# Performance work log

Hardware: AMD Instinct MI355X
Metric: run time of the kernel (lower is better)

Reference implementation:

```python
import jax, jax.numpy as jnp
import numpy as np

D_MODEL = 1024
D_FF = 4096
N_EXPERTS = 8
TOP_K = 2
TEMP = 0.7
B, L = 4, 2048


def setup_inputs() -> dict:
    key = jax.random.key(0)
    ks = jax.random.split(key, 6)
    s = 0.02  # init scale
    return {
        "x": jax.random.normal(ks[0], (B, L, D_MODEL), jnp.float32),
        "Wr": jax.random.normal(ks[1], (D_MODEL, N_EXPERTS), jnp.float32) * s,
        "br": jnp.zeros((N_EXPERTS,), jnp.float32),
        "W1": jax.random.normal(ks[2], (N_EXPERTS, D_MODEL, D_FF), jnp.float32) * s,
        "b1": jnp.zeros((N_EXPERTS, D_FF), jnp.float32),
        "W2": jax.random.normal(ks[3], (N_EXPERTS, D_FF, D_MODEL), jnp.float32) * s,
        "b2": jnp.zeros((N_EXPERTS, D_MODEL), jnp.float32),
    }


def reference(x, Wr, br, W1, b1, W2, b2):
    # Eval-mode MoE: no router jitter, dropout is identity.
    Bb, Ll, Dd = x.shape
    E = Wr.shape[1]
    xf = x.reshape(-1, Dd)                              # [T, D]
    T = xf.shape[0]

    logits = xf @ Wr + br                               # [T, E]
    probs = jax.nn.softmax(logits / TEMP, axis=-1)      # [T, E]
    top_w, top_i = jax.lax.top_k(probs, TOP_K)          # [T, K]
    top_w = top_w / (jnp.sum(top_w, axis=-1, keepdims=True) + 1e-6)

    # Per-token per-expert combine weight (zero for non-selected experts).
    cw = jnp.zeros((T, E), xf.dtype).at[jnp.arange(T)[:, None], top_i].add(top_w)

    out = jnp.zeros_like(xf)
    for e in range(E):  # small fixed expert loop
        h = jax.nn.silu(xf @ W1[e] + b1[e])             # [T, d_ff]
        out = out + cw[:, e:e + 1] * (h @ W2[e] + b2[e])

    # Load-balance aux loss.
    counts = jnp.zeros((E,), xf.dtype).at[top_i.reshape(-1)].add(1.0)
    f_i = counts / T
    P_i = probs.mean(axis=0)
    aux = E * jnp.sum(f_i * P_i)
    return out.reshape(Bb, Ll, Dd), aux[None]
```

## Files before the change

kernel.cpp:

```cpp
#include <hip/hip_runtime.h>

#define DM     1024
#define DFF    4096
#define NE     8
#define TT     8192
#define CAP    8192
#define RTOK   32
#define MAXRA  17664

typedef __bf16 bf16x8 __attribute__((ext_vector_type(8)));
typedef float  f32x4  __attribute__((ext_vector_type(4)));
typedef unsigned short u16;
typedef unsigned int   u32;

__device__ __forceinline__ u16 f2bf(float f) {
    u32 u = __builtin_bit_cast(u32, f);
    u += 0x7fffu + ((u >> 16) & 1u);
    return (u16)(u >> 16);
}

__device__ __forceinline__ void gload_lds16(const void* g, void* l) {
    __builtin_amdgcn_global_load_lds(
        (const __attribute__((address_space(1))) void*)g,
        (__attribute__((address_space(3))) void*)l,
        16, 0, 0);
}

__global__ __launch_bounds__(256) void router_k(
    const float* __restrict__ x, const float* __restrict__ Wr, const float* __restrict__ br,
    int* __restrict__ expert_count, float* __restrict__ prob_sum,
    int* __restrict__ list_token, float* __restrict__ list_w,
    int* __restrict__ tok_e, int* __restrict__ tok_q, float* __restrict__ tok_w)
{
    __shared__ float wrT[NE][DM];
    __shared__ float ps[NE];
    __shared__ int   lcount[NE];
    __shared__ int   lbase[NE];
    __shared__ int   lexp[RTOK * 2];
    __shared__ float lw[RTOK * 2];
    __shared__ int   lslot[RTOK * 2];

    int tid = threadIdx.x;
    if (tid < NE) { ps[tid] = 0.f; lcount[tid] = 0; }
#pragma unroll
    for (int it = 0; it < 8; ++it) {
        int f = tid * 4 + it * 1024;
        float4 v = *reinterpret_cast<const float4*>(Wr + f);
        int e0 = f & 7, k = f >> 3;
        wrT[e0][k] = v.x; wrT[e0 + 1][k] = v.y; wrT[e0 + 2][k] = v.z; wrT[e0 + 3][k] = v.w;
    }
    __syncthreads();

    int w = tid >> 6, l = tid & 63;
    for (int j = 0; j < RTOK / 4; ++j) {
        int ti = w * (RTOK / 4) + j;
        int token = blockIdx.x * RTOK + ti;
        const float* xr = x + (size_t)token * DM;
        float acc[NE];
#pragma unroll
        for (int e = 0; e < NE; ++e) acc[e] = 0.f;
#pragma unroll
        for (int i = 0; i < 4; ++i) {
            float4 xv = *reinterpret_cast<const float4*>(xr + i * 256 + l * 4);
#pragma unroll
            for (int e = 0; e < NE; ++e) {
                float4 wv = *reinterpret_cast<const float4*>(&wrT[e][i * 256 + l * 4]);
                acc[e] += xv.x * wv.x + xv.y * wv.y + xv.z * wv.z + xv.w * wv.w;
            }
        }
#pragma unroll
        for (int off = 32; off >= 1; off >>= 1) {
#pragma unroll
            for (int e = 0; e < NE; ++e) acc[e] += __shfl_xor(acc[e], off);
        }
        if (l == 0) {
            float li[NE], m = -1e30f;
#pragma unroll
            for (int e = 0; e < NE; ++e) { li[e] = (acc[e] + br[e]) * (1.0f / 0.7f); m = fmaxf(m, li[e]); }
            float p[NE], s = 0.f;
#pragma unroll
            for (int e = 0; e < NE; ++e) { p[e] = __expf(li[e] - m); s += p[e]; }
            float inv = 1.f / s;
#pragma unroll
            for (int e = 0; e < NE; ++e) { p[e] *= inv; atomicAdd(&ps[e], p[e]); }
            float v1 = -1.f, v2 = -1.f; int e1 = 0, e2 = 0;
#pragma unroll
            for (int e = 0; e < NE; ++e) {
                float pe = p[e];
                if (pe > v1)      { v2 = v1; e2 = e1; v1 = pe; e1 = e; }
                else if (pe > v2) { v2 = pe; e2 = e; }
            }
            float denom = v1 + v2 + 1e-6f;
            lexp[2 * ti]     = e1; lw[2 * ti]     = v1 / denom; lslot[2 * ti]     = atomicAdd(&lcount[e1], 1);
            lexp[2 * ti + 1] = e2; lw[2 * ti + 1] = v2 / denom; lslot[2 * ti + 1] = atomicAdd(&lcount[e2], 1);
        }
    }
    __syncthreads();
    if (tid < NE) {
        lbase[tid] = atomicAdd(&expert_count[tid], lcount[tid]);
        atomicAdd(&prob_sum[tid], ps[tid]);
    }
    __syncthreads();
    if (tid < RTOK * 2) {
        int e = lexp[tid];
        int q = lbase[e] + lslot[tid];
        int token = blockIdx.x * RTOK + (tid >> 1);
        list_token[e * CAP + q] = token;
        list_w[e * CAP + q] = lw[tid];
        int slot = token * 2 + (tid & 1);
        tok_e[slot] = e; tok_q[slot] = q; tok_w[slot] = lw[tid];
    }
}

__global__ void scan_aux_k(const int* __restrict__ expert_count, const float* __restrict__ prob_sum,
                           int* __restrict__ padded_count, int* __restrict__ poffsets,
                           float* __restrict__ aux_out)
{
    if (threadIdx.x == 0 && blockIdx.x == 0) {
        int off = 0; float aux = 0.f;
        for (int e = 0; e < NE; ++e) {
            int c = expert_count[e];
            int pc = (c + 127) / 128 * 128;
            poffsets[e] = off; padded_count[e] = pc; off += pc;
            aux += ((float)c / (float)TT) * (prob_sum[e] / (float)TT);
        }
        aux_out[0] = aux * (float)NE;
    }
}

__global__ __launch_bounds__(256) void gather_k(
    const float* __restrict__ x, const int* __restrict__ list_token,
    const int* __restrict__ expert_count, const int* __restrict__ padded_count,
    const int* __restrict__ poffsets, u16* __restrict__ Xg)
{
    int e = blockIdx.y;
    int p0 = blockIdx.x * 8;
    if (p0 >= padded_count[e]) return;
    int tid = threadIdx.x;
    int rr = tid >> 5, cl = tid & 31;
    int p = p0 + rr;
    int g = poffsets[e] + p;
    u16* dst = Xg + (size_t)g * DM;
    bool valid = p < expert_count[e];
    int tok = valid ? list_token[e * CAP + p] : 0;
    const float* src = x + (size_t)tok * DM;
#pragma unroll
    for (int i = 0; i < 4; ++i) {
        int c0 = cl * 8 + i * 256;
        uint4 v;
        if (valid) {
            float4 f0 = *reinterpret_cast<const float4*>(src + c0);
            float4 f1 = *reinterpret_cast<const float4*>(src + c0 + 4);
            v.x = f2bf(f0.x) | ((u32)f2bf(f0.y) << 16);
            v.y = f2bf(f0.z) | ((u32)f2bf(f0.w) << 16);
            v.z = f2bf(f1.x) | ((u32)f2bf(f1.y) << 16);
            v.w = f2bf(f1.z) | ((u32)f2bf(f1.w) << 16);
        } else {
            v.x = 0; v.y = 0; v.z = 0; v.w = 0;
        }
        *reinterpret_cast<uint4*>(dst + c0) = v;
    }
}

__global__ __launch_bounds__(256) void convt_k(
    const float* __restrict__ src, u16* __restrict__ dst, int rs, int Ktot, long dstEStride)
{
    __shared__ float tile[64][65];
    int e = blockIdx.z;
    int k0 = blockIdx.x * 64, j0 = blockIdx.y * 64;
    const float* s = src + (size_t)e * 4194304;
    int tid = threadIdx.x;
    {
        int jj = (tid & 15) * 4, kb = tid >> 4;
#pragma unroll
        for (int i = 0; i < 4; ++i) {
            int k = kb + i * 16;
            float4 v = *reinterpret_cast<const float4*>(s + (size_t)(k0 + k) * rs + j0 + jj);
            tile[k][jj] = v.x; tile[k][jj + 1] = v.y; tile[k][jj + 2] = v.z; tile[k][jj + 3] = v.w;
        }
    }
    __syncthreads();
    {
        int kk = (tid & 15) * 4, jb = tid >> 4;
        u16* d = dst + (size_t)e * dstEStride;
#pragma unroll
        for (int i = 0; i < 4; ++i) {
            int j = jb + i * 16;
            uint2 q;
            q.x = f2bf(tile[kk][j])     | ((u32)f2bf(tile[kk + 1][j]) << 16);
            q.y = f2bf(tile[kk + 2][j]) | ((u32)f2bf(tile[kk + 3][j]) << 16);
            *reinterpret_cast<uint2*>(d + (size_t)(j0 + j) * Ktot + k0 + kk) = q;
        }
    }
}

__device__ __forceinline__ void stage_tile(const u16* __restrict__ rows, long lda, int kt, char* buf) {
    int tid = threadIdx.x;
    int w = tid >> 6, l = tid & 63;
#pragma unroll
    for (int i = 0; i < 4; ++i) {
        int sbase = i * 256 + w * 64;
        int sl = sbase + l;
        int row = sl >> 3;
        int c8 = (sl & 7) ^ (row & 7);
        const u16* src = rows + (size_t)row * lda + kt * 64 + c8 * 8;
        gload_lds16(src, buf + sbase * 16);
    }
}

__device__ __forceinline__ void gemm_main(
    const u16* __restrict__ Arows, long lda,
    const u16* __restrict__ Brows, long ldb,
    int nkt, char* smem, f32x4 acc[4][4])
{
    int tid = threadIdx.x;
    int l = tid & 63, lane16 = l & 15, hi = l >> 4;
    int wm = (tid >> 6) & 1, wn = tid >> 7;

    for (int kt = 0; kt < nkt; ++kt) {
        stage_tile(Arows, lda, kt, smem);
        stage_tile(Brows, ldb, kt, smem + 16384);
        __syncthreads();
        const char* bufA = smem;
        const char* bufB = smem + 16384;
#pragma unroll
        for (int kk = 0; kk < 2; ++kk) {
            bf16x8 af[4], bb[4];
#pragma unroll
            for (int mi = 0; mi < 4; ++mi) {
                int row = wm * 64 + mi * 16 + lane16;
                int ch = (kk * 4 + hi) ^ (row & 7);
                af[mi] = *reinterpret_cast<const bf16x8*>(bufA + (row * 8 + ch) * 16);
            }
#pragma unroll
            for (int ni = 0; ni < 4; ++ni) {
                int row = wn * 64 + ni * 16 + lane16;
                int ch = (kk * 4 + hi) ^ (row & 7);
                bb[ni] = *reinterpret_cast<const bf16x8*>(bufB + (row * 8 + ch) * 16);
            }
#pragma unroll
            for (int mi = 0; mi < 4; ++mi)
#pragma unroll
                for (int ni = 0; ni < 4; ++ni)
                    acc[mi][ni] = __builtin_amdgcn_mfma_f32_16x16x32_bf16(af[mi], bb[ni], acc[mi][ni], 0, 0, 0);
        }
        __syncthreads();
    }
}

__global__ __launch_bounds__(256, 4) void gemm1_k(
    const u16* __restrict__ Xg, const u16* __restrict__ W1c, const float* __restrict__ b1,
    const int* __restrict__ padded_count, const int* __restrict__ poffsets,
    u16* __restrict__ H)
{
    __shared__ char smem[32768];
    int n = blockIdx.x;
    int e = n >> 11, r11 = n & 2047;
    int g = r11 >> 8;
    int rb = g * 8 + ((r11 >> 5) & 7);
    int cb = r11 & 31;
    if (rb * 128 >= padded_count[e]) return;
    int row0 = poffsets[e] + rb * 128;
    const u16* Arows = Xg + (size_t)row0 * 1024;
    const u16* Brows = W1c + (size_t)e * DFF * 1024 + (size_t)cb * 128 * 1024;
    f32x4 acc[4][4];
#pragma unroll
    for (int i = 0; i < 4; ++i)
#pragma unroll
        for (int j = 0; j < 4; ++j) { acc[i][j][0]=0.f; acc[i][j][1]=0.f; acc[i][j][2]=0.f; acc[i][j][3]=0.f; }
    gemm_main(Arows, 1024, Brows, 1024, 16, smem, acc);

    int tid = threadIdx.x;
    int l = tid & 63, lane16 = l & 15, hi = l >> 4;
    int wm = (tid >> 6) & 1, wn = tid >> 7;
    const float* b1e = b1 + (size_t)e * DFF;
#pragma unroll
    for (int mi = 0; mi < 4; ++mi) {
#pragma unroll
        for (int ni = 0; ni < 4; ++ni) {
            int col = cb * 128 + wn * 64 + ni * 16 + lane16;
            float bv = b1e[col];
#pragma unroll
            for (int r = 0; r < 4; ++r) {
                int grow = row0 + wm * 64 + mi * 16 + hi * 4 + r;
                float z = acc[mi][ni][r] + bv;
                float hval = z / (1.f + __expf(-z));
                H[(size_t)grow * DFF + col] = f2bf(hval);
            }
        }
    }
}

__global__ __launch_bounds__(256, 4) void gemm2_k(
    const u16* __restrict__ Hb, const u16* __restrict__ W2c,
    const int* __restrict__ padded_count, const int* __restrict__ poffsets,
    float* __restrict__ Og)
{
    __shared__ char smem[32768];
    int n = blockIdx.x;
    int e = n >> 9, r9 = n & 511;
    int g = r9 >> 7;
    int rb = g * 16 + ((r9 >> 3) & 15);
    int cb = r9 & 7;
    if (rb * 128 >= padded_count[e]) return;
    int row0 = poffsets[e] + rb * 128;
    const u16* Arows = Hb + (size_t)row0 * DFF;
    const u16* Brows = W2c + (size_t)e * DM * DFF + (size_t)cb * 128 * DFF;
    f32x4 acc[4][4];
#pragma unroll
    for (int i = 0; i < 4; ++i)
#pragma unroll
        for (int j = 0; j < 4; ++j) { acc[i][j][0]=0.f; acc[i][j][1]=0.f; acc[i][j][2]=0.f; acc[i][j][3]=0.f; }
    gemm_main(Arows, DFF, Brows, DFF, 64, smem, acc);

    int tid = threadIdx.x;
    int l = tid & 63, lane16 = l & 15, hi = l >> 4;
    int wm = (tid >> 6) & 1, wn = tid >> 7;
#pragma unroll
    for (int mi = 0; mi < 4; ++mi) {
#pragma unroll
        for (int r = 0; r < 4; ++r) {
            int grow = row0 + wm * 64 + mi * 16 + hi * 4 + r;
            float* orow = Og + (size_t)grow * DM;
#pragma unroll
            for (int ni = 0; ni < 4; ++ni) {
                int col = cb * 128 + wn * 64 + ni * 16 + lane16;
                orow[col] = acc[mi][ni][r];
            }
        }
    }
}

__global__ __launch_bounds__(256) void combine_k(
    const float* __restrict__ Og, const float* __restrict__ b2,
    const int* __restrict__ tok_e, const int* __restrict__ tok_q, const float* __restrict__ tok_w,
    const int* __restrict__ poffsets, float* __restrict__ out)
{
    int t = blockIdx.x * 4 + (threadIdx.x >> 6);
    int l = threadIdx.x & 63;
    int e0 = tok_e[t * 2], q0 = tok_q[t * 2];
    int e1 = tok_e[t * 2 + 1], q1 = tok_q[t * 2 + 1];
    float w0 = tok_w[t * 2], w1 = tok_w[t * 2 + 1];
    const float* r0 = Og + (size_t)(poffsets[e0] + q0) * DM;
    const float* r1 = Og + (size_t)(poffsets[e1] + q1) * DM;
    const float* bb0 = b2 + (size_t)e0 * DM;
    const float* bb1 = b2 + (size_t)e1 * DM;
    float* o = out + (size_t)t * DM;
#pragma unroll
    for (int i = 0; i < 4; ++i) {
        int c = l * 4 + i * 256;
        float4 a = *reinterpret_cast<const float4*>(r0 + c);
        float4 b = *reinterpret_cast<const float4*>(r1 + c);
        float4 p = *reinterpret_cast<const float4*>(bb0 + c);
        float4 q = *reinterpret_cast<const float4*>(bb1 + c);
        float4 res;
        res.x = w0 * (a.x + p.x) + w1 * (b.x + q.x);
        res.y = w0 * (a.y + p.y) + w1 * (b.y + q.y);
        res.z = w0 * (a.z + p.z) + w1 * (b.z + q.z);
        res.w = w0 * (a.w + p.w) + w1 * (b.w + q.w);
        *reinterpret_cast<float4*>(o + c) = res;
    }
}

extern "C" void kernel_launch(void* const* d_in, const int* in_sizes, int n_in,
                              void* d_out, int out_size, void* d_ws, size_t ws_size,
                              hipStream_t stream) {
    (void)in_sizes; (void)n_in; (void)out_size; (void)ws_size;
    const float* x  = (const float*)d_in[0];
    const float* Wr = (const float*)d_in[1];
    const float* br = (const float*)d_in[2];
    const float* W1 = (const float*)d_in[3];
    const float* b1 = (const float*)d_in[4];
    const float* W2 = (const float*)d_in[5];
    const float* b2 = (const float*)d_in[6];
    float* out = (float*)d_out;

    char* ws = (char*)d_ws;
    int*   expert_count = (int*)(ws + 0);
    float* prob_sum     = (float*)(ws + 32);
    int*   padded_count = (int*)(ws + 64);
    int*   poffsets     = (int*)(ws + 96);
    int*   list_token   = (int*)(ws + 256);
    float* list_w       = (float*)(ws + 256 + 262144);
    int*   tok_e        = (int*)(ws + 524544);
    int*   tok_q        = (int*)(ws + 524544 + 65536);
    float* tok_w        = (float*)(ws + 524544 + 131072);

    const size_t HDR    = 1048576;
    const size_t OFF_HB = HDR;
    const size_t OFF_W2 = OFF_HB + (size_t)MAXRA * DFF * 2;
    const size_t OFF_XG = OFF_W2 + (size_t)NE * DM * DFF * 2;
    const size_t OFF_W1 = OFF_XG + (size_t)MAXRA * DM * 2;
    u16*   Hb  = (u16*)(ws + OFF_HB);
    u16*   W2c = (u16*)(ws + OFF_W2);
    u16*   Xg  = (u16*)(ws + OFF_XG);
    u16*   W1c = (u16*)(ws + OFF_W1);
    float* Og  = (float*)(ws + OFF_XG);

    hipMemsetAsync(ws, 0, 64, stream);
    router_k<<<TT / RTOK, 256, 0, stream>>>(x, Wr, br, expert_count, prob_sum, list_token, list_w,
                                            tok_e, tok_q, tok_w);
    scan_aux_k<<<1, 64, 0, stream>>>(expert_count, prob_sum, padded_count, poffsets,
                                     out + (size_t)TT * DM);
    gather_k<<<dim3(1024, 8), 256, 0, stream>>>(x, list_token, expert_count, padded_count, poffsets, Xg);

    convt_k<<<dim3(16, 64, 8), 256, 0, stream>>>(W1, W1c, DFF, 1024, (long)DM * DFF);
    convt_k<<<dim3(64, 16, 8), 256, 0, stream>>>(W2, W2c, DM, 4096, (long)DM * DFF);

    gemm1_k<<<16384, 256, 0, stream>>>(Xg, W1c, b1, padded_count, poffsets, Hb);
    gemm2_k<<<4096, 256, 0, stream>>>(Hb, W2c, padded_count, poffsets, Og);
    combine_k<<<TT / 4, 256, 0, stream>>>(Og, b2, tok_e, tok_q, tok_w, poffsets, out);
}
```

Baseline: 537.4 us.

## Switch expert GEMMs to 32x32x16 MFMA with 256x128 block tiles

Replaces the 16x16x32 MFMA inner loop with 32x32x16 MFMA instructions. The block tile grows from 128x128 to 256x128, with each wave computing 128x64, which raises operand reuse per LDS read and per global load. The grouped 1D block swizzle becomes a plain 3D grid (col block, row block, expert), and the epilogue gains bounds checks against the padded count. In exchange it uses more LDS and registers (launch bounds drop to 2 blocks per SM), wastes more work on padded rows, and loses the L2-friendly block ordering.

```diff
diff --git a/kernel.cpp b/kernel.cpp
--- a/kernel.cpp
+++ b/kernel.cpp
@@ -9,7 +9,7 @@
 #define MAXRA  17664
 
 typedef __bf16 bf16x8 __attribute__((ext_vector_type(8)));
-typedef float  f32x4  __attribute__((ext_vector_type(4)));
+typedef float  f32x16 __attribute__((ext_vector_type(16)));
 typedef unsigned short u16;
 typedef unsigned int   u32;
 
@@ -194,138 +194,144 @@
     }
 }
 
-__device__ __forceinline__ void stage_tile(const u16* __restrict__ rows, long lda, int kt, char* buf) {
+
+__device__ __forceinline__ f32x16 mfma32(bf16x8 a, bf16x8 b, f32x16 c) {
+    return __builtin_amdgcn_mfma_f32_32x32x16_bf16(a, b, c, 0, 0, 0);
+}
+
+__device__ __forceinline__ void gemm_main32(
+    const u16* __restrict__ A, long lda, const u16* __restrict__ B, long ldb,
+    int nkt, char* smem, f32x16 acc[4][2])
+{
     int tid = threadIdx.x;
-    int w = tid >> 6, l = tid & 63;
-#pragma unroll
-    for (int i = 0; i < 4; ++i) {
-        int sbase = i * 256 + w * 64;
-        int sl = sbase + l;
-        int row = sl >> 3;
-        int c8 = (sl & 7) ^ (row & 7);
-        const u16* src = rows + (size_t)row * lda + kt * 64 + c8 * 8;
-        gload_lds16(src, buf + sbase * 16);
-    }
-}
-
-__device__ __forceinline__ void gemm_main(
-    const u16* __restrict__ Arows, long lda,
-    const u16* __restrict__ Brows, long ldb,
-    int nkt, char* smem, f32x4 acc[4][4])
-{
-    int tid = threadIdx.x;
-    int l = tid & 63, lane16 = l & 15, hi = l >> 4;
-    int wm = (tid >> 6) & 1, wn = tid >> 7;
+    int l = tid & 63, l31 = l & 31, kg = l >> 5;
+    int wid = tid >> 6, wm = wid >> 1, wn = wid & 1;
+    char* bufA = smem;
+    char* bufB = smem + 32768;
 
     for (int kt = 0; kt < nkt; ++kt) {
-        stage_tile(Arows, lda, kt, smem);
-        stage_tile(Brows, ldb, kt, smem + 16384);
+#pragma unroll
+        for (int i = 0; i < 8; ++i) {
+            int sbase = i * 256 + wid * 64;
+            int sl = sbase + l;
+            int row = sl >> 3;
+            int c8 = (sl & 7) ^ (row & 7);
+            gload_lds16(A + (size_t)row * lda + kt * 64 + c8 * 8, bufA + sbase * 16);
+        }
+#pragma unroll
+        for (int i = 0; i < 4; ++i) {
+            int sbase = i * 256 + wid * 64;
+            int sl = sbase + l;
+            int row = sl >> 3;
+            int c8 = (sl & 7) ^ (row & 7);
+            gload_lds16(B + (size_t)row * ldb + kt * 64 + c8 * 8, bufB + sbase * 16);
+        }
         __syncthreads();
-        const char* bufA = smem;
-        const char* bufB = smem + 16384;
-#pragma unroll
-        for (int kk = 0; kk < 2; ++kk) {
-            bf16x8 af[4], bb[4];
+#pragma unroll
+        for (int ks = 0; ks < 4; ++ks) {
+            bf16x8 af[4], bb[2];
 #pragma unroll
             for (int mi = 0; mi < 4; ++mi) {
-                int row = wm * 64 + mi * 16 + lane16;
-                int ch = (kk * 4 + hi) ^ (row & 7);
+                int row = wm * 128 + mi * 32 + l31;
+                int ch = (ks * 2 + kg) ^ (row & 7);
                 af[mi] = *reinterpret_cast<const bf16x8*>(bufA + (row * 8 + ch) * 16);
             }
 #pragma unroll
-            for (int ni = 0; ni < 4; ++ni) {
-                int row = wn * 64 + ni * 16 + lane16;
-                int ch = (kk * 4 + hi) ^ (row & 7);
+            for (int ni = 0; ni < 2; ++ni) {
+                int row = wn * 64 + ni * 32 + l31;
+                int ch = (ks * 2 + kg) ^ (row & 7);
                 bb[ni] = *reinterpret_cast<const bf16x8*>(bufB + (row * 8 + ch) * 16);
             }
 #pragma unroll
             for (int mi = 0; mi < 4; ++mi)
 #pragma unroll
-                for (int ni = 0; ni < 4; ++ni)
-                    acc[mi][ni] = __builtin_amdgcn_mfma_f32_16x16x32_bf16(af[mi], bb[ni], acc[mi][ni], 0, 0, 0);
+                for (int ni = 0; ni < 2; ++ni)
+                    acc[mi][ni] = mfma32(af[mi], bb[ni], acc[mi][ni]);
         }
         __syncthreads();
     }
 }
 
-__global__ __launch_bounds__(256, 4) void gemm1_k(
+__global__ __launch_bounds__(256, 2) void gemm1_k(
     const u16* __restrict__ Xg, const u16* __restrict__ W1c, const float* __restrict__ b1,
     const int* __restrict__ padded_count, const int* __restrict__ poffsets,
     u16* __restrict__ H)
 {
-    __shared__ char smem[32768];
-    int n = blockIdx.x;
-    int e = n >> 11, r11 = n & 2047;
-    int g = r11 >> 8;
-    int rb = g * 8 + ((r11 >> 5) & 7);
-    int cb = r11 & 31;
-    if (rb * 128 >= padded_count[e]) return;
-    int row0 = poffsets[e] + rb * 128;
+    __shared__ char smem[49152];
+    int cb = blockIdx.x, rb = blockIdx.y, e = blockIdx.z;
+    int pc = padded_count[e];
+    if (rb * 256 >= pc) return;
+    int row0 = poffsets[e] + rb * 256;
     const u16* Arows = Xg + (size_t)row0 * 1024;
     const u16* Brows = W1c + (size_t)e * DFF * 1024 + (size_t)cb * 128 * 1024;
-    f32x4 acc[4][4];
+    f32x16 acc[4][2];
 #pragma unroll
     for (int i = 0; i < 4; ++i)
 #pragma unroll
-        for (int j = 0; j < 4; ++j) { acc[i][j][0]=0.f; acc[i][j][1]=0.f; acc[i][j][2]=0.f; acc[i][j][3]=0.f; }
-    gemm_main(Arows, 1024, Brows, 1024, 16, smem, acc);
-
-    int tid = threadIdx.x;
-    int l = tid & 63, lane16 = l & 15, hi = l >> 4;
-    int wm = (tid >> 6) & 1, wn = tid >> 7;
+        for (int j = 0; j < 2; ++j)
+#pragma unroll
+            for (int r = 0; r < 16; ++r) acc[i][j][r] = 0.f;
+    gemm_main32(Arows, 1024, Brows, 1024, 16, smem, acc);
+
+    int tid = threadIdx.x, l = tid & 63, l31 = l & 31, kg = l >> 5;
+    int wid = tid >> 6, wm = wid >> 1, wn = wid & 1;
     const float* b1e = b1 + (size_t)e * DFF;
 #pragma unroll
     for (int mi = 0; mi < 4; ++mi) {
 #pragma unroll
-        for (int ni = 0; ni < 4; ++ni) {
-            int col = cb * 128 + wn * 64 + ni * 16 + lane16;
+        for (int ni = 0; ni < 2; ++ni) {
+            int col = cb * 128 + wn * 64 + ni * 32 + l31;
             float bv = b1e[col];
 #pragma unroll
-            for (int r = 0; r < 4; ++r) {
-                int grow = row0 + wm * 64 + mi * 16 + hi * 4 + r;
-                float z = acc[mi][ni][r] + bv;
-                float hval = z / (1.f + __expf(-z));
-                H[(size_t)grow * DFF + col] = f2bf(hval);
-            }
-        }
-    }
-}
-
-__global__ __launch_bounds__(256, 4) void gemm2_k(
+            for (int reg = 0; reg < 16; ++reg) {
+                int rl = wm * 128 + mi * 32 + (reg & 3) + 8 * (reg >> 2) + 4 * kg;
+                int p = rb * 256 + rl;
+                if (p < pc) {
+                    float z = acc[mi][ni][reg] + bv;
+                    float hval = z / (1.f + __expf(-z));
+                    H[(size_t)(row0 + rl) * DFF + col] = f2bf(hval);
+                }
+            }
+        }
+    }
+}
+
+__global__ __launch_bounds__(256, 2) void gemm2_k(
     const u16* __restrict__ Hb, const u16* __restrict__ W2c,
     const int* __restrict__ padded_count, const int* __restrict__ poffsets,
     float* __restrict__ Og)
 {
-    __shared__ char smem[32768];
-    int n = blockIdx.x;
-    int e = n >> 9, r9 = n & 511;
-    int g = r9 >> 7;
-    int rb = g * 16 + ((r9 >> 3) & 15);
-    int cb = r9 & 7;
-    if (rb * 128 >= padded_count[e]) return;
-    int row0 = poffsets[e] + rb * 128;
+    __shared__ char smem[49152];
+    int cb = blockIdx.x, rb = blockIdx.y, e = blockIdx.z;
+    int pc = padded_count[e];
+    if (rb * 256 >= pc) return;
+    int row0 = poffsets[e] + rb * 256;
     const u16* Arows = Hb + (size_t)row0 * DFF;
     const u16* Brows = W2c + (size_t)e * DM * DFF + (size_t)cb * 128 * DFF;
-    f32x4 acc[4][4];
+    f32x16 acc[4][2];
 #pragma unroll
     for (int i = 0; i < 4; ++i)
 #pragma unroll
-        for (int j = 0; j < 4; ++j) { acc[i][j][0]=0.f; acc[i][j][1]=0.f; acc[i][j][2]=0.f; acc[i][j][3]=0.f; }
-    gemm_main(Arows, DFF, Brows, DFF, 64, smem, acc);
-
-    int tid = threadIdx.x;
-    int l = tid & 63, lane16 = l & 15, hi = l >> 4;
-    int wm = (tid >> 6) & 1, wn = tid >> 7;
+        for (int j = 0; j < 2; ++j)
+#pragma unroll
+            for (int r = 0; r < 16; ++r) acc[i][j][r] = 0.f;
+    gemm_main32(Arows, DFF, Brows, DFF, 64, smem, acc);
+
+    int tid = threadIdx.x, l = tid & 63, l31 = l & 31, kg = l >> 5;
+    int wid = tid >> 6, wm = wid >> 1, wn = wid & 1;
 #pragma unroll
     for (int mi = 0; mi < 4; ++mi) {
 #pragma unroll
-        for (int r = 0; r < 4; ++r) {
-            int grow = row0 + wm * 64 + mi * 16 + hi * 4 + r;
-            float* orow = Og + (size_t)grow * DM;
-#pragma unroll
-            for (int ni = 0; ni < 4; ++ni) {
-                int col = cb * 128 + wn * 64 + ni * 16 + lane16;
-                orow[col] = acc[mi][ni][r];
+        for (int reg = 0; reg < 16; ++reg) {
+            int rl = wm * 128 + mi * 32 + (reg & 3) + 8 * (reg >> 2) + 4 * kg;
+            int p = rb * 256 + rl;
+            if (p < pc) {
+                float* orow = Og + (size_t)(row0 + rl) * DM;
+#pragma unroll
+                for (int ni = 0; ni < 2; ++ni) {
+                    int col = cb * 128 + wn * 64 + ni * 32 + l31;
+                    orow[col] = acc[mi][ni][reg];
+                }
             }
         }
     }
@@ -407,7 +413,7 @@
     convt_k<<<dim3(16, 64, 8), 256, 0, stream>>>(W1, W1c, DFF, 1024, (long)DM * DFF);
     convt_k<<<dim3(64, 16, 8), 256, 0, stream>>>(W2, W2c, DM, 4096, (long)DM * DFF);
 
-    gemm1_k<<<16384, 256, 0, stream>>>(Xg, W1c, b1, padded_count, poffsets, Hb);
-    gemm2_k<<<4096, 256, 0, stream>>>(Hb, W2c, padded_count, poffsets, Og);
+    gemm1_k<<<dim3(32, 33, 8), 256, 0, stream>>>(Xg, W1c, b1, padded_count, poffsets, Hb);
+    gemm2_k<<<dim3(8, 33, 8), 256, 0, stream>>>(Hb, W2c, padded_count, poffsets, Og);
     combine_k<<<TT / 4, 256, 0, stream>>>(Og, b2, tok_e, tok_q, tok_w, poffsets, out);
 }
```

Measured after the change: 675.4 us. 25.7% more time.
